# Kernel tuning notes

Hardware: AMD Instinct MI355X
Metric: run time of the kernel (lower is better)

The kernel has to match this reference:

```python
import jax, jax.numpy as jnp
import numpy as np

N, F_IN, HEADS, D_HEAD, HID, OUT, E = 50000, 128, 4, 64, 256, 2, 800000
NEG_SLOPE = 0.2


def setup_inputs() -> dict:
    key = jax.random.key(0)
    ks = jax.random.split(key, 12)
    x = jax.random.normal(ks[0], (N, F_IN), dtype=jnp.float32)
    edge_index = jax.random.randint(ks[1], (2, E), 0, N, dtype=jnp.int64)
    s = 0.05
    W_gat = jax.random.normal(ks[2], (F_IN, HEADS * D_HEAD), dtype=jnp.float32) * s
    att_src = jax.random.normal(ks[3], (HEADS, D_HEAD), dtype=jnp.float32) * s
    att_dst = jax.random.normal(ks[4], (HEADS, D_HEAD), dtype=jnp.float32) * s
    b_gat = jnp.zeros((HEADS * D_HEAD,), dtype=jnp.float32)
    W1 = jax.random.normal(ks[5], (HEADS * D_HEAD, HID), dtype=jnp.float32) * s
    b1 = jnp.zeros((HID,), dtype=jnp.float32)
    W2 = jax.random.normal(ks[6], (HID, HID), dtype=jnp.float32) * s
    b2 = jnp.zeros((HID,), dtype=jnp.float32)
    W3 = jax.random.normal(ks[7], (HID, OUT), dtype=jnp.float32) * s
    b3 = jnp.zeros((OUT,), dtype=jnp.float32)
    return {"x": x, "edge_index": edge_index, "W_gat": W_gat, "att_src": att_src,
            "att_dst": att_dst, "b_gat": b_gat, "W1": W1, "b1": b1,
            "W2": W2, "b2": b2, "W3": W3, "b3": b3}


def _gat(x, edge_index, W_gat, att_src, att_dst, b_gat):
    n = x.shape[0]
    loop = jnp.arange(n, dtype=edge_index.dtype)
    src = jnp.concatenate([edge_index[0], loop])  # [E+N] message sources j
    dst = jnp.concatenate([edge_index[1], loop])  # [E+N] message targets i
    h = (x @ W_gat).reshape(n, HEADS, D_HEAD)      # [N,H,D]
    a_s = jnp.einsum('nhd,hd->nh', h, att_src)     # [N,H]
    a_d = jnp.einsum('nhd,hd->nh', h, att_dst)     # [N,H]
    e = a_s[src] + a_d[dst]                        # [E',H]
    e = jax.nn.leaky_relu(e, NEG_SLOPE)
    # per-destination-node softmax over incoming edges (numerically stable)
    emax = jax.ops.segment_max(e, dst, num_segments=n)
    e = jnp.exp(e - emax[dst])
    denom = jax.ops.segment_sum(e, dst, num_segments=n)
    alpha = e / denom[dst]                         # [E',H]
    msg = h[src] * alpha[:, :, None]               # [E',H,D]
    out = jax.ops.segment_sum(msg, dst, num_segments=n)  # [N,H,D]
    return out.reshape(n, HEADS * D_HEAD) + b_gat


def reference(x, edge_index, W_gat, att_src, att_dst, b_gat, W1, b1, W2, b2, W3, b3):
    h = _gat(x, edge_index, W_gat, att_src, att_dst, b_gat)
    h = jax.nn.relu(h @ W1 + b1)
    h = jax.nn.relu(h @ W2 + b2)
    return h @ W3 + b3
```

## Files before the change

### kernel.cpp

```cpp
#include <hip/hip_runtime.h>
#include <math.h>

#define N_NODES 50000
#define NP 50048
#define F_IN 128
#define HD 256
#define HID 256
#define NE 800000
#define CAP 64
#define NEG_SLOPE 0.2f

#define G1_BLOCKS (NP / 64)
#define FILL_BLOCKS ((NE + 1023) / 1024)

typedef __attribute__((ext_vector_type(8))) __bf16 bf16x8;
typedef __attribute__((ext_vector_type(4))) __bf16 bf16x4;
typedef __attribute__((ext_vector_type(4))) float f32x4;

#define GLD_LDS16(g, l)                                                      \
    __builtin_amdgcn_global_load_lds(                                        \
        (const __attribute__((address_space(1))) unsigned int*)(g),          \
        (__attribute__((address_space(3))) unsigned int*)(l), 16, 0, 0)

__device__ __forceinline__ void tile_transpose(const float* __restrict__ W,
                                               __bf16* __restrict__ Wt,
                                               int K, int M, int k0, int m0, int t) {
    __shared__ float tile[64][65];
#pragma unroll
    for (int i = 0; i < 4; ++i) {
        int row = i * 16 + (t >> 4);
        int col = (t & 15) * 4;
        float4 v = *(const float4*)&W[(size_t)(k0 + row) * M + m0 + col];
        tile[row][col] = v.x; tile[row][col + 1] = v.y;
        tile[row][col + 2] = v.z; tile[row][col + 3] = v.w;
    }
    __syncthreads();
#pragma unroll
    for (int i = 0; i < 4; ++i) {
        int mrow = i * 16 + (t >> 4);
        int kcol = (t & 15) * 4;
        bf16x4 o = {(__bf16)tile[kcol][mrow], (__bf16)tile[kcol + 1][mrow],
                    (__bf16)tile[kcol + 2][mrow], (__bf16)tile[kcol + 3][mrow]};
        *(bf16x4*)&Wt[(size_t)(m0 + mrow) * K + k0 + kcol] = o;
    }
}

#define PB_WG 8
#define PB_W1 16
#define PB_W2 16

__global__ __launch_bounds__(256) void prep_kernel(const float* __restrict__ Wg,
                                                   const float* __restrict__ W1,
                                                   const float* __restrict__ W2,
                                                   __bf16* __restrict__ Wg_t,
                                                   __bf16* __restrict__ W1_t,
                                                   __bf16* __restrict__ W2_t) {
    int b = blockIdx.x, t = threadIdx.x;
    if (b < PB_WG) {
        tile_transpose(Wg, Wg_t, F_IN, HD, (b >> 2) * 64, (b & 3) * 64, t);
    } else if (b < PB_WG + PB_W1) {
        int tt = b - PB_WG;
        tile_transpose(W1, W1_t, HD, HID, (tt >> 2) * 64, (tt & 3) * 64, t);
    } else {
        int tt = b - PB_WG - PB_W1;
        tile_transpose(W2, W2_t, HID, HID, (tt >> 2) * 64, (tt & 3) * 64, t);
    }
}

__global__ __launch_bounds__(256) void g1_fill_kernel(const float* __restrict__ x,
                                                      const __bf16* __restrict__ Bt,
                                                      const float* __restrict__ att_src,
                                                      const float* __restrict__ att_dst,
                                                      const int* __restrict__ ew,
                                                      __bf16* __restrict__ h,
                                                      float* __restrict__ a_s,
                                                      float* __restrict__ a_d,
                                                      int* __restrict__ cnt,
                                                      unsigned short* __restrict__ bucket) {
    __shared__ __bf16 As[64 * 32];
    __shared__ __bf16 Bs[256 * 32];

    if (blockIdx.x >= G1_BLOCKS) {
        int e0 = (blockIdx.x - G1_BLOCKS) * 1024 + threadIdx.x;
        int hi = ew[2 * e0 + 1];
        unsigned long long bal = __ballot(hi != 0);
        const bool is64 = (bal == 0);
        int ee[4], ss[4], dd[4], pos[4];
        int cnt_local = 0;
#pragma unroll
        for (int i = 0; i < 4; ++i) {
            int e = e0 + i * 256;
            if (e < NE) {
                int src, dst;
                if (is64) { src = ew[2 * e]; dst = ew[2 * NE + 2 * e]; }
                else      { src = ew[e];     dst = ew[NE + e]; }
                ee[cnt_local] = e; ss[cnt_local] = src; dd[cnt_local] = dst;
                ++cnt_local;
            }
        }
#pragma unroll
        for (int i = 0; i < 4; ++i)
            if (i < cnt_local) pos[i] = atomicAdd(&cnt[dd[i]], 1);
#pragma unroll
        for (int i = 0; i < 4; ++i)
            if (i < cnt_local && pos[i] < CAP - 1)
                bucket[dd[i] * CAP + pos[i]] = (unsigned short)ss[i];
        return;
    }

    const int t = threadIdx.x;
    const int lane = t & 63, wv = t >> 6;
    const int lr = lane & 15, q = lane >> 4, lk = q * 8;
    const int col_off = wv * 64;
    const int row0 = blockIdx.x * 64;
    const int sr = t >> 2, sk = (t & 3) * 8;
    const int arow = row0 + sr;
    const bool avalid = arow < N_NODES;

    f32x4 acc[4][4];
#pragma unroll
    for (int r = 0; r < 4; ++r)
#pragma unroll
        for (int c = 0; c < 4; ++c) acc[r][c] = f32x4{0.f, 0.f, 0.f, 0.f};

    for (int k0 = 0; k0 < F_IN; k0 += 32) {
        float4 v0 = {0, 0, 0, 0}, v1 = {0, 0, 0, 0};
        if (avalid) {
            const float* xp = &x[(size_t)arow * F_IN + k0 + sk];
            v0 = *(const float4*)xp;
            v1 = *(const float4*)(xp + 4);
        }
        bf16x8 o;
        o[0] = (__bf16)v0.x; o[1] = (__bf16)v0.y; o[2] = (__bf16)v0.z; o[3] = (__bf16)v0.w;
        o[4] = (__bf16)v1.x; o[5] = (__bf16)v1.y; o[6] = (__bf16)v1.z; o[7] = (__bf16)v1.w;
        *(bf16x8*)&As[sr * 32 + sk] = o;
#pragma unroll
        for (int s = 0; s < 4; ++s) {
            int r = s * 64 + sr;
            GLD_LDS16(&Bt[(size_t)r * F_IN + k0 + sk], &Bs[r * 32 + sk]);
        }
        __syncthreads();
        bf16x8 af[4], bfr[4];
#pragma unroll
        for (int i = 0; i < 4; ++i) {
            af[i]  = *(const bf16x8*)&As[(i * 16 + lr) * 32 + lk];
            bfr[i] = *(const bf16x8*)&Bs[(col_off + i * 16 + lr) * 32 + lk];
        }
#pragma unroll
        for (int r = 0; r < 4; ++r)
#pragma unroll
            for (int c = 0; c < 4; ++c)
                acc[r][c] = __builtin_amdgcn_mfma_f32_16x16x32_bf16(af[r], bfr[c], acc[r][c], 0, 0, 0);
        __syncthreads();
    }

    float asv[4], adv[4];
#pragma unroll
    for (int c = 0; c < 4; ++c) {
        int col = col_off + c * 16 + lr;
        asv[c] = att_src[col];
        adv[c] = att_dst[col];
    }
    float ps[4][4], pd[4][4];
#pragma unroll
    for (int r = 0; r < 4; ++r)
#pragma unroll
        for (int i = 0; i < 4; ++i) { ps[r][i] = 0.f; pd[r][i] = 0.f; }

#pragma unroll
    for (int c = 0; c < 4; ++c) {
        int col = col_off + c * 16 + lr;
#pragma unroll
        for (int r = 0; r < 4; ++r) {
#pragma unroll
            for (int i = 0; i < 4; ++i) {
                int row = row0 + r * 16 + q * 4 + i;
                float v = acc[r][c][i];
                h[(size_t)row * HD + col] = (__bf16)v;
                ps[r][i] += v * asv[c];
                pd[r][i] += v * adv[c];
            }
        }
    }
#pragma unroll
    for (int r = 0; r < 4; ++r)
#pragma unroll
        for (int i = 0; i < 4; ++i) {
#pragma unroll
            for (int m = 1; m < 16; m <<= 1) {
                ps[r][i] += __shfl_xor(ps[r][i], m);
                pd[r][i] += __shfl_xor(pd[r][i], m);
            }
        }
    if (lr == 0) {
#pragma unroll
        for (int r = 0; r < 4; ++r)
#pragma unroll
            for (int i = 0; i < 4; ++i) {
                int row = row0 + r * 16 + q * 4 + i;
                a_s[row * 4 + wv] = ps[r][i];
                a_d[row * 4 + wv] = pd[r][i];
            }
    }
}

__device__ __forceinline__ float lrelu(float v) { return v >= 0.f ? v : NEG_SLOPE * v; }

__global__ __launch_bounds__(128) void gat_aggregate_kernel(const __bf16* __restrict__ h,
                                                            const float* __restrict__ a_s,
                                                            const float* __restrict__ a_d,
                                                            const int* __restrict__ cnt,
                                                            const unsigned short* __restrict__ bucket,
                                                            const float* __restrict__ b_gat,
                                                            __bf16* __restrict__ gat) {
    __shared__ unsigned short s_src[2][64];
    __shared__ float s_alpha[2][64][4];
    const int lane = threadIdx.x & 63;
    const int wv = threadIdx.x >> 6;
    const int n = blockIdx.x * 2 + wv;

    int deg_e = cnt[n];
    if (deg_e > CAP - 1) deg_e = CAP - 1;
    const int deg = deg_e + 1;
    int src = n;
    float4 e = {-1e30f, -1e30f, -1e30f, -1e30f};
    float4 ad = *(const float4*)&a_d[n * 4];
    if (lane < deg) {
        if (lane < deg_e) src = bucket[n * CAP + lane];
        float4 as4 = *(const float4*)&a_s[src * 4];
        e.x = lrelu(as4.x + ad.x);
        e.y = lrelu(as4.y + ad.y);
        e.z = lrelu(as4.z + ad.z);
        e.w = lrelu(as4.w + ad.w);
    }
    float4 m = e;
#pragma unroll
    for (int off = 1; off < 64; off <<= 1) {
        m.x = fmaxf(m.x, __shfl_xor(m.x, off));
        m.y = fmaxf(m.y, __shfl_xor(m.y, off));
        m.z = fmaxf(m.z, __shfl_xor(m.z, off));
        m.w = fmaxf(m.w, __shfl_xor(m.w, off));
    }
    float4 wgt = {0, 0, 0, 0};
    if (lane < deg) {
        wgt.x = __expf(e.x - m.x); wgt.y = __expf(e.y - m.y);
        wgt.z = __expf(e.z - m.z); wgt.w = __expf(e.w - m.w);
    }
    float4 s = wgt;
#pragma unroll
    for (int off = 1; off < 64; off <<= 1) {
        s.x += __shfl_xor(s.x, off); s.y += __shfl_xor(s.y, off);
        s.z += __shfl_xor(s.z, off); s.w += __shfl_xor(s.w, off);
    }
    s_src[wv][lane] = (unsigned short)src;
    s_alpha[wv][lane][0] = wgt.x / s.x;
    s_alpha[wv][lane][1] = wgt.y / s.y;
    s_alpha[wv][lane][2] = wgt.z / s.z;
    s_alpha[wv][lane][3] = wgt.w / s.w;

    const int half = lane >> 5;
    const int l32 = lane & 31;
    const int c0 = l32 * 8;
    const int head = l32 >> 3;
    float acc[8];
#pragma unroll
    for (int k = 0; k < 8; ++k) acc[k] = 0.f;

    const int mde = (deg + 1) & ~1;
    int j = 0;
    for (; j + 8 <= mde; j += 8) {
        int j0 = j + half, j1 = j + 2 + half, j2 = j + 4 + half, j3 = j + 6 + half;
        int s0 = s_src[wv][j0], s1 = s_src[wv][j1];
        int s2 = s_src[wv][j2], s3 = s_src[wv][j3];
        float a0 = s_alpha[wv][j0][head], a1 = s_alpha[wv][j1][head];
        float a2 = s_alpha[wv][j2][head], a3 = s_alpha[wv][j3][head];
        bf16x8 h0 = *(const bf16x8*)&h[(size_t)s0 * HD + c0];
        bf16x8 h1 = *(const bf16x8*)&h[(size_t)s1 * HD + c0];
        bf16x8 h2 = *(const bf16x8*)&h[(size_t)s2 * HD + c0];
        bf16x8 h3 = *(const bf16x8*)&h[(size_t)s3 * HD + c0];
#pragma unroll
        for (int k = 0; k < 8; ++k)
            acc[k] += a0 * (float)h0[k] + a1 * (float)h1[k]
                    + a2 * (float)h2[k] + a3 * (float)h3[k];
    }
    for (; j < mde; j += 2) {
        int j0 = j + half;
        int s0 = s_src[wv][j0];
        float a0 = s_alpha[wv][j0][head];
        bf16x8 h0 = *(const bf16x8*)&h[(size_t)s0 * HD + c0];
#pragma unroll
        for (int k = 0; k < 8; ++k)
            acc[k] += a0 * (float)h0[k];
    }
#pragma unroll
    for (int k = 0; k < 8; ++k) acc[k] += __shfl_xor(acc[k], 32);

    if (half == 0) {
        float4 bg0 = *(const float4*)&b_gat[c0];
        float4 bg1 = *(const float4*)&b_gat[c0 + 4];
        bf16x8 o;
        o[0] = (__bf16)(acc[0] + bg0.x); o[1] = (__bf16)(acc[1] + bg0.y);
        o[2] = (__bf16)(acc[2] + bg0.z); o[3] = (__bf16)(acc[3] + bg0.w);
        o[4] = (__bf16)(acc[4] + bg1.x); o[5] = (__bf16)(acc[5] + bg1.y);
        o[6] = (__bf16)(acc[6] + bg1.z); o[7] = (__bf16)(acc[7] + bg1.w);
        *(bf16x8*)&gat[(size_t)n * HD + c0] = o;
    }
}

__global__ __launch_bounds__(256) void fused_mlp_kernel(const __bf16* __restrict__ A,
                                                        const __bf16* __restrict__ W1t,
                                                        const __bf16* __restrict__ W2t,
                                                        const float* __restrict__ b1,
                                                        const float* __restrict__ b2,
                                                        const float* __restrict__ W3,
                                                        const float* __restrict__ b3,
                                                        float* __restrict__ out) {
    __shared__ __bf16 As[64 * 32];
    __shared__ __bf16 Ws[256 * 32];
    __shared__ __bf16 h1s[8 * 64 * 32];
    __shared__ float s_out[64][2];
    const int t = threadIdx.x;
    const int lane = t & 63, wv = t >> 6;
    const int lr = lane & 15, q = lane >> 4, lk = q * 8;
    const int col_off = wv * 64;
    const int row0 = blockIdx.x * 64;
    const int sr = t >> 2, sk = (t & 3) * 8;

    if (t < 128) ((float*)s_out)[t] = 0.f;

    f32x4 acc[4][4];
#pragma unroll
    for (int r = 0; r < 4; ++r)
#pragma unroll
        for (int c = 0; c < 4; ++c) acc[r][c] = f32x4{0.f, 0.f, 0.f, 0.f};

    for (int k0 = 0; k0 < HD; k0 += 32) {
        GLD_LDS16(&A[(size_t)(row0 + sr) * HD + k0 + sk], &As[sr * 32 + sk]);
#pragma unroll
        for (int s = 0; s < 4; ++s) {
            int r = s * 64 + sr;
            GLD_LDS16(&W1t[(size_t)r * HD + k0 + sk], &Ws[r * 32 + sk]);
        }
        __syncthreads();
        bf16x8 af[4], bfr[4];
#pragma unroll
        for (int i = 0; i < 4; ++i) {
            af[i]  = *(const bf16x8*)&As[(i * 16 + lr) * 32 + lk];
            bfr[i] = *(const bf16x8*)&Ws[(col_off + i * 16 + lr) * 32 + lk];
        }
#pragma unroll
        for (int r = 0; r < 4; ++r)
#pragma unroll
            for (int c = 0; c < 4; ++c)
                acc[r][c] = __builtin_amdgcn_mfma_f32_16x16x32_bf16(af[r], bfr[c], acc[r][c], 0, 0, 0);
        __syncthreads();
    }
#pragma unroll
    for (int c = 0; c < 4; ++c) {
        int col = col_off + c * 16 + lr;
        float bv = b1[col];
        int cb = (col >> 5) * 2048;
        int kk = col & 31;
#pragma unroll
        for (int r = 0; r < 4; ++r)
#pragma unroll
            for (int i = 0; i < 4; ++i) {
                int row = r * 16 + q * 4 + i;
                float v = fmaxf(acc[r][c][i] + bv, 0.f);
                h1s[cb + row * 32 + kk] = (__bf16)v;
                acc[r][c][i] = 0.f;
            }
    }
    __syncthreads();

    for (int k0 = 0; k0 < HID; k0 += 32) {
#pragma unroll
        for (int s = 0; s < 4; ++s) {
            int r = s * 64 + sr;
            GLD_LDS16(&W2t[(size_t)r * HID + k0 + sk], &Ws[r * 32 + sk]);
        }
        __syncthreads();
        const int cb = (k0 >> 5) * 2048;
        bf16x8 af[4], bfr[4];
#pragma unroll
        for (int i = 0; i < 4; ++i) {
            af[i]  = *(const bf16x8*)&h1s[cb + (i * 16 + lr) * 32 + lk];
            bfr[i] = *(const bf16x8*)&Ws[(col_off + i * 16 + lr) * 32 + lk];
        }
#pragma unroll
        for (int r = 0; r < 4; ++r)
#pragma unroll
            for (int c = 0; c < 4; ++c)
                acc[r][c] = __builtin_amdgcn_mfma_f32_16x16x32_bf16(af[r], bfr[c], acc[r][c], 0, 0, 0);
        __syncthreads();
    }

    float b2v[4], w30[4], w31[4];
#pragma unroll
    for (int c = 0; c < 4; ++c) {
        int col = col_off + c * 16 + lr;
        b2v[c] = b2[col];
        w30[c] = W3[col * 2];
        w31[c] = W3[col * 2 + 1];
    }
#pragma unroll
    for (int r = 0; r < 4; ++r) {
#pragma unroll
        for (int i = 0; i < 4; ++i) {
            float o0 = 0.f, o1 = 0.f;
#pragma unroll
            for (int c = 0; c < 4; ++c) {
                float v = fmaxf(acc[r][c][i] + b2v[c], 0.f);
                o0 += v * w30[c];
                o1 += v * w31[c];
            }
#pragma unroll
            for (int m = 1; m < 16; m <<= 1) {
                o0 += __shfl_xor(o0, m);
                o1 += __shfl_xor(o1, m);
            }
            if (lr == 0) {
                int row = r * 16 + q * 4 + i;
                atomicAdd(&s_out[row][0], o0);
                atomicAdd(&s_out[row][1], o1);
            }
        }
    }
    __syncthreads();
    if (t < 128) {
        int row = t >> 1, o = t & 1;
        int g = row0 + row;
        if (g < N_NODES) out[g * 2 + o] = s_out[row][o] + b3[o];
    }
}

extern "C" void kernel_launch(void* const* d_in, const int* in_sizes, int n_in,
                              void* d_out, int out_size, void* d_ws, size_t ws_size,
                              hipStream_t stream) {
    const float* x       = (const float*)d_in[0];
    const int*   ei      = (const int*)d_in[1];
    const float* W_gat   = (const float*)d_in[2];
    const float* att_src = (const float*)d_in[3];
    const float* att_dst = (const float*)d_in[4];
    const float* b_gat   = (const float*)d_in[5];
    const float* W1      = (const float*)d_in[6];
    const float* b1      = (const float*)d_in[7];
    const float* W2      = (const float*)d_in[8];
    const float* b2      = (const float*)d_in[9];
    const float* W3      = (const float*)d_in[10];
    const float* b3      = (const float*)d_in[11];
    float* out = (float*)d_out;

    char* ws = (char*)d_ws;
    __bf16* h_bf   = (__bf16*)ws;  ws += (size_t)NP * HD * 2;
    __bf16* gat_bf = (__bf16*)ws;  ws += (size_t)NP * HD * 2;
    __bf16* Wg_t   = (__bf16*)ws;  ws += (size_t)HD * F_IN * 2;
    __bf16* W1_t   = (__bf16*)ws;  ws += (size_t)HID * HD * 2;
    __bf16* W2_t   = (__bf16*)ws;  ws += (size_t)HID * HID * 2;
    float* a_s     = (float*)ws;   ws += (size_t)NP * 4 * 4;
    float* a_d     = (float*)ws;   ws += (size_t)NP * 4 * 4;
    int* cnt       = (int*)ws;     ws += (size_t)N_NODES * 4;
    unsigned short* bucket = (unsigned short*)ws;
    ws += (size_t)N_NODES * CAP * 2;

    hipMemsetAsync(cnt, 0, (size_t)N_NODES * 4, stream);
    prep_kernel<<<PB_WG + PB_W1 + PB_W2, 256, 0, stream>>>(
        W_gat, W1, W2, Wg_t, W1_t, W2_t);
    g1_fill_kernel<<<G1_BLOCKS + FILL_BLOCKS, 256, 0, stream>>>(
        x, Wg_t, att_src, att_dst, ei, h_bf, a_s, a_d, cnt, bucket);
    gat_aggregate_kernel<<<N_NODES / 2, 128, 0, stream>>>(h_bf, a_s, a_d, cnt, bucket,
                                                          b_gat, gat_bf);
    fused_mlp_kernel<<<NP / 64, 256, 0, stream>>>(gat_bf, W1_t, W2_t, b1, b2, W3, b3, out);
}
```

Baseline: 255.1 us.

## Replace per-node global atomic bucketing with two-pass superblock binning via LDS

Edge bucketing now happens in two passes. First, each edge atomically appends a packed (local dst, src) word to a superblock of 64 destination nodes. A new kernel then sorts each superblock into per-node buckets in shared memory and writes them out with vector stores. This replaces scattered global atomics on 50k counters and scattered 2-byte stores, and drops the memset launch because the counters are zeroed inside prep. The cost is an extra kernel launch and intermediate traffic, and superblock overflow above 1280 edges would silently drop edges.

After: 391.0 us. 53.3% more time.

```diff
diff --git a/kernel.cpp b/kernel.cpp
--- a/kernel.cpp
+++ b/kernel.cpp
@@ -11,11 +11,14 @@
 #define NEG_SLOPE 0.2f
 
 #define G1_BLOCKS (NP / 64)
-#define FILL_BLOCKS ((NE + 1023) / 1024)
+#define P1_BLOCKS (NE / 256)
+#define NSB 782
+#define SB_CAP 1280
 
 typedef __attribute__((ext_vector_type(8))) __bf16 bf16x8;
 typedef __attribute__((ext_vector_type(4))) __bf16 bf16x4;
 typedef __attribute__((ext_vector_type(4))) float f32x4;
+typedef __attribute__((ext_vector_type(8))) unsigned short u16x8;
 
 #define GLD_LDS16(g, l)                                                      \
     __builtin_amdgcn_global_load_lds(                                        \
@@ -45,25 +48,15 @@
     }
 }
 
-#define PB_WG 8
-#define PB_W1 16
-#define PB_W2 16
-
 __global__ __launch_bounds__(256) void prep_kernel(const float* __restrict__ Wg,
-                                                   const float* __restrict__ W1,
-                                                   const float* __restrict__ W2,
                                                    __bf16* __restrict__ Wg_t,
-                                                   __bf16* __restrict__ W1_t,
-                                                   __bf16* __restrict__ W2_t) {
+                                                   int* __restrict__ scnt) {
     int b = blockIdx.x, t = threadIdx.x;
-    if (b < PB_WG) {
-        tile_transpose(Wg, Wg_t, F_IN, HD, (b >> 2) * 64, (b & 3) * 64, t);
-    } else if (b < PB_WG + PB_W1) {
-        int tt = b - PB_WG;
-        tile_transpose(W1, W1_t, HD, HID, (tt >> 2) * 64, (tt & 3) * 64, t);
+    if (b == 0) {
+        for (int i = t; i < NSB; i += 256) scnt[i] = 0;
     } else {
-        int tt = b - PB_WG - PB_W1;
-        tile_transpose(W2, W2_t, HID, HID, (tt >> 2) * 64, (tt & 3) * 64, t);
+        int tt = b - 1;
+        tile_transpose(Wg, Wg_t, F_IN, HD, (tt >> 2) * 64, (tt & 3) * 64, t);
     }
 }
 
@@ -75,36 +68,23 @@
                                                       __bf16* __restrict__ h,
                                                       float* __restrict__ a_s,
                                                       float* __restrict__ a_d,
-                                                      int* __restrict__ cnt,
-                                                      unsigned short* __restrict__ bucket) {
+                                                      int* __restrict__ scnt,
+                                                      unsigned* __restrict__ sedge) {
     __shared__ __bf16 As[64 * 32];
     __shared__ __bf16 Bs[256 * 32];
 
     if (blockIdx.x >= G1_BLOCKS) {
-        int e0 = (blockIdx.x - G1_BLOCKS) * 1024 + threadIdx.x;
-        int hi = ew[2 * e0 + 1];
+        int e = (blockIdx.x - G1_BLOCKS) * 256 + threadIdx.x;
+        int hi = ew[2 * e + 1];
         unsigned long long bal = __ballot(hi != 0);
-        const bool is64 = (bal == 0);
-        int ee[4], ss[4], dd[4], pos[4];
-        int cnt_local = 0;
-#pragma unroll
-        for (int i = 0; i < 4; ++i) {
-            int e = e0 + i * 256;
-            if (e < NE) {
-                int src, dst;
-                if (is64) { src = ew[2 * e]; dst = ew[2 * NE + 2 * e]; }
-                else      { src = ew[e];     dst = ew[NE + e]; }
-                ee[cnt_local] = e; ss[cnt_local] = src; dd[cnt_local] = dst;
-                ++cnt_local;
-            }
-        }
-#pragma unroll
-        for (int i = 0; i < 4; ++i)
-            if (i < cnt_local) pos[i] = atomicAdd(&cnt[dd[i]], 1);
-#pragma unroll
-        for (int i = 0; i < 4; ++i)
-            if (i < cnt_local && pos[i] < CAP - 1)
-                bucket[dd[i] * CAP + pos[i]] = (unsigned short)ss[i];
+        int src, dst;
+        if (bal == 0) { src = ew[2 * e]; dst = ew[2 * NE + 2 * e]; }
+        else          { src = ew[e];     dst = ew[NE + e]; }
+        int sb = dst >> 6;
+        int pos = atomicAdd(&scnt[sb], 1);
+        if (pos < SB_CAP)
+            sedge[(size_t)sb * SB_CAP + pos] =
+                ((unsigned)(dst & 63) << 16) | (unsigned)src;
         return;
     }
 
@@ -201,6 +181,48 @@
                 a_s[row * 4 + wv] = ps[r][i];
                 a_d[row * 4 + wv] = pd[r][i];
             }
+    }
+}
+
+__global__ __launch_bounds__(256) void fill2_kernel(const int* __restrict__ scnt,
+                                                    const unsigned* __restrict__ sedge,
+                                                    int* __restrict__ cnt,
+                                                    unsigned short* __restrict__ bucket,
+                                                    const float* __restrict__ W1,
+                                                    const float* __restrict__ W2,
+                                                    __bf16* __restrict__ W1_t,
+                                                    __bf16* __restrict__ W2_t) {
+    const int t = threadIdx.x;
+    if (blockIdx.x >= NSB) {
+        int b = blockIdx.x - NSB;
+        if (b < 16) tile_transpose(W1, W1_t, HD, HID, (b >> 2) * 64, (b & 3) * 64, t);
+        else { b -= 16; tile_transpose(W2, W2_t, HID, HID, (b >> 2) * 64, (b & 3) * 64, t); }
+        return;
+    }
+    __shared__ unsigned short lbuck[64 * 64];
+    __shared__ int lcnt[64];
+    const int sb = blockIdx.x;
+    if (t < 64) lcnt[t] = 0;
+    __syncthreads();
+    int m = scnt[sb];
+    if (m > SB_CAP) m = SB_CAP;
+    for (int i = t; i < m; i += 256) {
+        unsigned p = sedge[(size_t)sb * SB_CAP + i];
+        int dl = p >> 16;
+        int slot = atomicAdd(&lcnt[dl], 1);
+        if (slot < CAP - 1)
+            lbuck[dl * 64 + slot] = (unsigned short)(p & 0xffff);
+    }
+    __syncthreads();
+    const int n0 = sb * 64;
+    for (int i = t; i < 512; i += 256) {
+        int node = i >> 3, off = (i & 7) * 8;
+        *(u16x8*)&bucket[(size_t)(n0 + node) * CAP + off] =
+            *(const u16x8*)&lbuck[node * 64 + off];
+    }
+    if (t < 64 && n0 + t < N_NODES) {
+        int d = lcnt[t];
+        cnt[n0 + t] = d > CAP - 1 ? CAP - 1 : d;
     }
 }
 
@@ -462,12 +484,15 @@
     int* cnt       = (int*)ws;     ws += (size_t)N_NODES * 4;
     unsigned short* bucket = (unsigned short*)ws;
     ws += (size_t)N_NODES * CAP * 2;
-
-    hipMemsetAsync(cnt, 0, (size_t)N_NODES * 4, stream);
-    prep_kernel<<<PB_WG + PB_W1 + PB_W2, 256, 0, stream>>>(
-        W_gat, W1, W2, Wg_t, W1_t, W2_t);
-    g1_fill_kernel<<<G1_BLOCKS + FILL_BLOCKS, 256, 0, stream>>>(
-        x, Wg_t, att_src, att_dst, ei, h_bf, a_s, a_d, cnt, bucket);
+    int* scnt      = (int*)ws;     ws += (size_t)NSB * 4;
+    unsigned* sedge = (unsigned*)ws;
+    ws += (size_t)NSB * SB_CAP * 4;
+
+    prep_kernel<<<9, 256, 0, stream>>>(W_gat, Wg_t, scnt);
+    g1_fill_kernel<<<G1_BLOCKS + P1_BLOCKS, 256, 0, stream>>>(
+        x, Wg_t, att_src, att_dst, ei, h_bf, a_s, a_d, scnt, sedge);
+    fill2_kernel<<<NSB + 32, 256, 0, stream>>>(scnt, sedge, cnt, bucket,
+                                               W1, W2, W1_t, W2_t);
     gat_aggregate_kernel<<<N_NODES / 2, 128, 0, stream>>>(h_bf, a_s, a_d, cnt, bucket,
                                                           b_gat, gat_bf);
     fused_mlp_kernel<<<NP / 64, 256, 0, stream>>>(gat_bf, W1_t, W2_t, b1, b2, W3, b3, out);
```
